# Kernel optimization log

Measured on AMD Instinct MI355X. Metric: run time of the kernel, lower is better.

## Reference

```python
import jax, jax.numpy as jnp
import numpy as np

N_NODES = 50000
N_EDGES = 300000
F_IN, HID, N_CLS = 256, 256, 128


def _glorot_linear(key, fan_in, fan_out):
    # torch.nn.Linear-style uniform init, kaiming bound 1/sqrt(fan_in)
    s = 1.0 / np.sqrt(fan_in)
    return jax.random.uniform(key, (fan_in, fan_out), jnp.float32, -s, s)


def setup_inputs() -> dict:
    key = jax.random.key(0)
    ks = jax.random.split(key, 8)
    x = jax.random.normal(ks[0], (N_NODES, F_IN), jnp.float32)
    edge_index = jax.random.randint(ks[1], (2, N_EDGES), 0, N_NODES, dtype=jnp.int32)
    return {
        "x": x,
        "edge_index": edge_index,
        "W1": _glorot_linear(ks[2], F_IN, HID), "b1": jnp.zeros((HID,), jnp.float32),
        "W2": _glorot_linear(ks[3], HID, HID),  "b2": jnp.zeros((HID,), jnp.float32),
        "W3": _glorot_linear(ks[4], HID, HID),  "b3": jnp.zeros((HID,), jnp.float32),
        "W4": _glorot_linear(ks[5], HID, N_CLS), "b4": jnp.zeros((N_CLS,), jnp.float32),
    }


def _gcn_conv(x, W, b, src, dst, norm, n):
    # x' = D^{-1/2} (A + I) D^{-1/2} X W + b   (PyG GCNConv default)
    h = x @ W                                  # [N, out]
    msg = h[src] * norm[:, None]               # gather + edge scaling  [E', out]
    return jax.ops.segment_sum(msg, dst, num_segments=n) + b


def reference(x, edge_index, W1, b1, W2, b2, W3, b3, W4, b4):
    n = x.shape[0]
    loops = jnp.arange(n, dtype=edge_index.dtype)
    src = jnp.concatenate([edge_index[0], loops])  # add self-loops
    dst = jnp.concatenate([edge_index[1], loops])
    # symmetric normalization: deg over target nodes (unit edge weights)
    deg = jax.ops.segment_sum(jnp.ones_like(dst, jnp.float32), dst, num_segments=n)
    dis = jnp.where(deg > 0, jax.lax.rsqrt(jnp.maximum(deg, 1.0)), 0.0)
    norm = dis[src] * dis[dst]                     # [E']

    h = jax.nn.relu(_gcn_conv(x, W1, b1, src, dst, norm, n))
    h = jax.nn.relu(_gcn_conv(h, W2, b2, src, dst, norm, n))
    h = jax.nn.relu(_gcn_conv(h, W3, b3, src, dst, norm, n))
    h = _gcn_conv(h, W4, b4, src, dst, norm, n)    # [N, C]

    # global_add_pool with batch == zeros -> single-graph sum pool
    pooled = jnp.sum(h, axis=0, keepdims=True)     # [1, C]
    return (pooled, jax.nn.log_softmax(pooled, axis=1))
```

## Files before the change

kernel.cpp:

```cpp
#include <hip/hip_runtime.h>


typedef __attribute__((ext_vector_type(8))) short short8;
typedef __attribute__((ext_vector_type(4))) float float4v;

__device__ __forceinline__ unsigned short f2b(float f) {
    unsigned int u = __builtin_bit_cast(unsigned int, f);
    u += 0x7fffu + ((u >> 16) & 1u);
    return (unsigned short)(u >> 16);
}
__device__ __forceinline__ float b2f(unsigned short b) {
    unsigned int u = ((unsigned int)b) << 16;
    return __builtin_bit_cast(float, u);
}


__global__ void zero_kernel(int* __restrict__ cnt, float* __restrict__ tsum,
                            float* __restrict__ acc, int N) {
    int i = blockIdx.x * 256 + threadIdx.x;
    if (i < N) { cnt[i] = 0; tsum[i] = 0.f; }
    if (i < 256) acc[i] = 0.f;
}

__global__ void count_kernel(const int* __restrict__ dst, int* __restrict__ cnt, int E) {
    int i = blockIdx.x * blockDim.x + threadIdx.x;
    if (i < E) atomicAdd(&cnt[dst[i]], 1);
}

__global__ void blocksum_kernel(const int* __restrict__ cnt, int* __restrict__ bsum, int N) {
    __shared__ int s[256];
    int t = threadIdx.x;
    int i = blockIdx.x * 256 + t;
    s[t] = (i < N) ? cnt[i] : 0;
    __syncthreads();
    for (int d = 128; d > 0; d >>= 1) {
        if (t < d) s[t] += s[t + d];
        __syncthreads();
    }
    if (t == 0) bsum[blockIdx.x] = s[0];
}

__global__ void bscan_kernel(int* __restrict__ bsum, int B) {
    __shared__ int s[256];
    int t = threadIdx.x;
    int v = (t < B) ? bsum[t] : 0;
    s[t] = v;
    __syncthreads();
    for (int d = 1; d < 256; d <<= 1) {
        int x = (t >= d) ? s[t - d] : 0;
        __syncthreads();
        s[t] += x;
        __syncthreads();
    }
    if (t < B) bsum[t] = s[t] - v;
}

__global__ void finalize_kernel(const int* __restrict__ cnt, const int* __restrict__ bsum,
                                int* __restrict__ offs, int* __restrict__ cursor,
                                float* __restrict__ dis, int N, int E) {
    __shared__ int s[256];
    int t = threadIdx.x;
    int i = blockIdx.x * 256 + t;
    int c = (i < N) ? cnt[i] : 0;
    s[t] = c;
    __syncthreads();
    for (int d = 1; d < 256; d <<= 1) {
        int x = (t >= d) ? s[t - d] : 0;
        __syncthreads();
        s[t] += x;
        __syncthreads();
    }
    if (i < N) {
        int ex = bsum[blockIdx.x] + s[t] - c;
        offs[i] = ex;
        cursor[i] = ex;
        dis[i] = rsqrtf((float)(c + 1));
    }
    if (blockIdx.x == 0 && t == 0) offs[N] = E;
}

__global__ void scatter_outsum_kernel(const int* __restrict__ src, const int* __restrict__ dst,
                                      const float* __restrict__ dis, int* __restrict__ cursor,
                                      int* __restrict__ csr_src, float* __restrict__ csr_nrm,
                                      float* __restrict__ tsum, int E) {
    int i = blockIdx.x * blockDim.x + threadIdx.x;
    if (i < E) {
        int s = src[i], d = dst[i];
        float dd = dis[d];
        int pos = atomicAdd(&cursor[d], 1);
        csr_src[pos] = s;
        csr_nrm[pos] = dis[s] * dd;
        atomicAdd(&tsum[s], dd);
    }
}


__global__ void convert_wt_kernel(const float* __restrict__ W1, const float* __restrict__ W2,
                                  const float* __restrict__ W3, unsigned short* __restrict__ Wt1,
                                  unsigned short* __restrict__ Wt2, unsigned short* __restrict__ Wt3) {
    const float* W = (blockIdx.y == 0) ? W1 : (blockIdx.y == 1) ? W2 : W3;
    unsigned short* Wt = (blockIdx.y == 0) ? Wt1 : (blockIdx.y == 1) ? Wt2 : Wt3;
    int n = blockIdx.x;
    int k = threadIdx.x;
    Wt[n * 256 + k] = f2b(W[k * 256 + n]);
}

template <int AFP32>
__global__ __launch_bounds__(512, 4) void gemm_bf16_kernel(
        const void* __restrict__ Ap, const unsigned short* __restrict__ Wt,
        unsigned short* __restrict__ C, int M) {
    __shared__ __align__(16) unsigned char smem[65536];
    unsigned short* As = (unsigned short*)smem;
    unsigned short* Bs = (unsigned short*)(smem + 128 * 72 * 2);
    const int tid = threadIdx.x;
    const int lane = tid & 63;
    const int wave = tid >> 6;
    const int l15 = lane & 15;
    const int quad = lane >> 4;
    const int wm = wave & 1;
    const int wn = wave >> 1;
    const int m0 = blockIdx.x * 128;

    float4v acc[4][4] = {};

    const int srow = tid >> 3;
    const int skof = (tid & 7) * 8;

    for (int kk = 0; kk < 256; kk += 64) {
#pragma unroll
        for (int p = 0; p < 2; p++) {
            int row = p * 64 + srow;
            int gm = m0 + row;
            if (AFP32) {
                const float* Af = (const float*)Ap;
                float4 lo = make_float4(0.f, 0.f, 0.f, 0.f);
                float4 hi = make_float4(0.f, 0.f, 0.f, 0.f);
                if (gm < M) {
                    lo = *(const float4*)&Af[(size_t)gm * 256 + kk + skof];
                    hi = *(const float4*)&Af[(size_t)gm * 256 + kk + skof + 4];
                }
                union { unsigned short u[8]; float4 v; } pk;
                pk.u[0] = f2b(lo.x); pk.u[1] = f2b(lo.y);
                pk.u[2] = f2b(lo.z); pk.u[3] = f2b(lo.w);
                pk.u[4] = f2b(hi.x); pk.u[5] = f2b(hi.y);
                pk.u[6] = f2b(hi.z); pk.u[7] = f2b(hi.w);
                *(float4*)&As[row * 72 + skof] = pk.v;
            } else {
                const unsigned short* Ab = (const unsigned short*)Ap;
                float4 av = make_float4(0.f, 0.f, 0.f, 0.f);
                if (gm < M) av = *(const float4*)&Ab[(size_t)gm * 256 + kk + skof];
                *(float4*)&As[row * 72 + skof] = av;
            }
        }
#pragma unroll
        for (int p = 0; p < 4; p++) {
            int row = p * 64 + srow;
            float4 bv = *(const float4*)&Wt[(size_t)row * 256 + kk + skof];
            *(float4*)&Bs[row * 72 + skof] = bv;
        }
        __syncthreads();
#pragma unroll
        for (int ks = 0; ks < 64; ks += 32) {
            short8 af[4], bf[4];
#pragma unroll
            for (int mi = 0; mi < 4; mi++)
                af[mi] = *(const short8*)&As[(wm * 64 + mi * 16 + l15) * 72 + ks + quad * 8];
#pragma unroll
            for (int nj = 0; nj < 4; nj++)
                bf[nj] = *(const short8*)&Bs[(wn * 64 + nj * 16 + l15) * 72 + ks + quad * 8];
#pragma unroll
            for (int mi = 0; mi < 4; mi++)
#pragma unroll
                for (int nj = 0; nj < 4; nj++)
                    acc[mi][nj] = __builtin_amdgcn_mfma_f32_16x16x32_bf16(
                        af[mi], bf[nj], acc[mi][nj], 0, 0, 0);
        }
        __syncthreads();
    }

    unsigned short* Cs = (unsigned short*)smem;
#pragma unroll
    for (int mi = 0; mi < 4; mi++)
#pragma unroll
        for (int r = 0; r < 4; r++) {
            int row = wm * 64 + mi * 16 + quad * 4 + r;
#pragma unroll
            for (int nj = 0; nj < 4; nj++)
                Cs[row * 256 + wn * 64 + nj * 16 + l15] = f2b(acc[mi][nj][r]);
        }
    __syncthreads();
#pragma unroll
    for (int i = 0; i < 8; i++) {
        int g = i * 512 + tid;
        int row = g >> 5;
        int c8 = (g & 31) * 8;
        if (m0 + row < M)
            *(float4*)&C[(size_t)(m0 + row) * 256 + c8] = *(const float4*)&Cs[row * 256 + c8];
    }
}

template <int RELU, int POOL>
__global__ __launch_bounds__(256) void agg_bf16_kernel(
        const unsigned short* __restrict__ T, const float* __restrict__ bias,
        const int* __restrict__ offs, const int* __restrict__ csr_src,
        const float* __restrict__ csr_nrm, const float* __restrict__ dis,
        unsigned short* __restrict__ out, int N,
        const float* __restrict__ tsum, float* __restrict__ partial) {
    int hw = threadIdx.x >> 5;
    int l = threadIdx.x & 31;
    int v = blockIdx.x * 8 + hw;
    int f8 = l * 8;
    float a[8] = {};
    float wv = 0.f;
    if (v < N) {
        int beg = offs[v], end = offs[v + 1];
        float dv = dis[v];
        float w = dv * dv;
        {
            short8 hs = *(const short8*)&T[(size_t)v * 256 + f8];
#pragma unroll
            for (int i = 0; i < 8; i++) a[i] = w * b2f((unsigned short)hs[i]);
        }
        int e = beg;
        for (; e + 4 <= end; e += 4) {
            int s0 = csr_src[e],     s1 = csr_src[e + 1];
            int s2 = csr_src[e + 2], s3 = csr_src[e + 3];
            float n0 = csr_nrm[e],     n1 = csr_nrm[e + 1];
            float n2 = csr_nrm[e + 2], n3 = csr_nrm[e + 3];
            short8 h0 = *(const short8*)&T[(size_t)s0 * 256 + f8];
            short8 h1 = *(const short8*)&T[(size_t)s1 * 256 + f8];
            short8 h2 = *(const short8*)&T[(size_t)s2 * 256 + f8];
            short8 h3 = *(const short8*)&T[(size_t)s3 * 256 + f8];
#pragma unroll
            for (int i = 0; i < 8; i++)
                a[i] += n0 * b2f((unsigned short)h0[i]) + n1 * b2f((unsigned short)h1[i])
                      + n2 * b2f((unsigned short)h2[i]) + n3 * b2f((unsigned short)h3[i]);
        }
        for (; e < end; e++) {
            int s = csr_src[e];
            float nm = csr_nrm[e];
            short8 h = *(const short8*)&T[(size_t)s * 256 + f8];
#pragma unroll
            for (int i = 0; i < 8; i++) a[i] += nm * b2f((unsigned short)h[i]);
        }
        float4 bv0 = *(const float4*)&bias[f8];
        float4 bv1 = *(const float4*)&bias[f8 + 4];
        a[0] += bv0.x; a[1] += bv0.y; a[2] += bv0.z; a[3] += bv0.w;
        a[4] += bv1.x; a[5] += bv1.y; a[6] += bv1.z; a[7] += bv1.w;
        if (RELU) {
#pragma unroll
            for (int i = 0; i < 8; i++) a[i] = fmaxf(a[i], 0.f);
        }
        uint4 o;
        o.x = (unsigned int)f2b(a[0]) | ((unsigned int)f2b(a[1]) << 16);
        o.y = (unsigned int)f2b(a[2]) | ((unsigned int)f2b(a[3]) << 16);
        o.z = (unsigned int)f2b(a[4]) | ((unsigned int)f2b(a[5]) << 16);
        o.w = (unsigned int)f2b(a[6]) | ((unsigned int)f2b(a[7]) << 16);
        *(uint4*)&out[(size_t)v * 256 + f8] = o;
        if (POOL) wv = dv * (dv + tsum[v]);
    }
    if (POOL) {
        __shared__ float red[2048];
#pragma unroll
        for (int i = 0; i < 8; i++) red[i * 256 + hw * 32 + l] = wv * a[i];
        __syncthreads();
        for (int s = 4; s > 0; s >>= 1) {
            if (hw < s) {
#pragma unroll
                for (int i = 0; i < 8; i++)
                    red[i * 256 + hw * 32 + l] += red[i * 256 + (hw + s) * 32 + l];
            }
            __syncthreads();
        }
        int f = threadIdx.x;
        partial[(size_t)blockIdx.x * 256 + f] = red[(f & 7) * 256 + (f >> 3)];
    }
}

__global__ void wpool_reduce(const float* __restrict__ partial, float* __restrict__ acc, int P) {
    int f = threadIdx.x;
    float a = 0.f;
    for (int p = blockIdx.x; p < P; p += gridDim.x)
        a += partial[(size_t)p * 256 + f];
    atomicAdd(&acc[f], a);
}

__global__ void final_kernel(const float* __restrict__ acc, const float* __restrict__ W4,
                             const float* __restrict__ b4, float* __restrict__ out, int N) {
    __shared__ float red[128];
    int c = threadIdx.x;
    float p = (float)N * b4[c];
    for (int k = 0; k < 256; k++) p += acc[k] * W4[k * 128 + c];
    out[c] = p;
    red[c] = p;
    __syncthreads();
    for (int s = 64; s > 0; s >>= 1) {
        if (c < s) red[c] = fmaxf(red[c], red[c + s]);
        __syncthreads();
    }
    float m = red[0];
    __syncthreads();
    red[c] = expf(p - m);
    __syncthreads();
    for (int s = 64; s > 0; s >>= 1) {
        if (c < s) red[c] += red[c + s];
        __syncthreads();
    }
    float lse = m + logf(red[0]);
    out[128 + c] = p - lse;
}

extern "C" void kernel_launch(void* const* d_in, const int* in_sizes, int n_in,
                              void* d_out, int out_size, void* d_ws, size_t ws_size,
                              hipStream_t stream) {
    const float* x  = (const float*)d_in[0];
    const int*   ei = (const int*)d_in[1];
    const float* W1 = (const float*)d_in[2];
    const float* b1 = (const float*)d_in[3];
    const float* W2 = (const float*)d_in[4];
    const float* b2 = (const float*)d_in[5];
    const float* W3 = (const float*)d_in[6];
    const float* b3 = (const float*)d_in[7];
    const float* W4 = (const float*)d_in[8];
    const float* b4 = (const float*)d_in[9];

    const int N = in_sizes[0] / 256;
    const int E = in_sizes[1] / 2;
    const int* src = ei;
    const int* dst = ei + E;

    char* p = (char*)d_ws;
    auto alloc = [&](size_t bytes) {
        char* r = p;
        p += (bytes + 255) & ~(size_t)255;
        return r;
    };
    int ab = (N + 7) / 8;

    int*            cnt     = (int*)alloc((size_t)N * 4);
    int*            offs    = (int*)alloc((size_t)(N + 1) * 4);
    int*            cursor  = (int*)alloc((size_t)N * 4);
    float*          dis     = (float*)alloc((size_t)N * 4);
    float*          tsum    = (float*)alloc((size_t)N * 4);
    int*            bsum    = (int*)alloc(1024 * 4);
    int*            csr_src = (int*)alloc((size_t)E * 4);
    float*          csr_nrm = (float*)alloc((size_t)E * 4);
    unsigned short* Wt1     = (unsigned short*)alloc(256 * 256 * 2);
    unsigned short* Wt2     = (unsigned short*)alloc(256 * 256 * 2);
    unsigned short* Wt3     = (unsigned short*)alloc(256 * 256 * 2);
    unsigned short* T       = (unsigned short*)alloc((size_t)N * 256 * 2);
    unsigned short* Abuf    = (unsigned short*)alloc((size_t)N * 256 * 2);
    float*          partial = (float*)alloc((size_t)ab * 256 * 4);
    float*          accbuf  = (float*)alloc(256 * 4);

    int eb = (E + 255) / 256;
    int nb = (N + 255) / 256;
    zero_kernel<<<nb, 256, 0, stream>>>(cnt, tsum, accbuf, N);
    count_kernel<<<eb, 256, 0, stream>>>(dst, cnt, E);
    blocksum_kernel<<<nb, 256, 0, stream>>>(cnt, bsum, N);
    bscan_kernel<<<1, 256, 0, stream>>>(bsum, nb);
    finalize_kernel<<<nb, 256, 0, stream>>>(cnt, bsum, offs, cursor, dis, N, E);
    scatter_outsum_kernel<<<eb, 256, 0, stream>>>(src, dst, dis, cursor, csr_src,
                                                  csr_nrm, tsum, E);

    convert_wt_kernel<<<dim3(256, 3), 256, 0, stream>>>(W1, W2, W3, Wt1, Wt2, Wt3);

    int ggrid = (N + 127) / 128;
    gemm_bf16_kernel<1><<<ggrid, 512, 0, stream>>>(x, Wt1, T, N);
    agg_bf16_kernel<1, 0><<<ab, 256, 0, stream>>>(T, b1, offs, csr_src, csr_nrm, dis,
                                                  Abuf, N, nullptr, nullptr);
    gemm_bf16_kernel<0><<<ggrid, 512, 0, stream>>>(Abuf, Wt2, T, N);
    agg_bf16_kernel<1, 0><<<ab, 256, 0, stream>>>(T, b2, offs, csr_src, csr_nrm, dis,
                                                  Abuf, N, nullptr, nullptr);
    gemm_bf16_kernel<0><<<ggrid, 512, 0, stream>>>(Abuf, Wt3, T, N);
    agg_bf16_kernel<1, 1><<<ab, 256, 0, stream>>>(T, b3, offs, csr_src, csr_nrm, dis,
                                                  Abuf, N, tsum, partial);

    wpool_reduce<<<64, 256, 0, stream>>>(partial, accbuf, ab);
    final_kernel<<<1, 128, 0, stream>>>(accbuf, W4, b4, (float*)d_out, N);
}
```

Measured before the change: 351.2 us.

## Split GEMM over N into 128x128 tiles with 256-thread blocks and direct stores

The GEMM now tiles the output as 128x128 per block, adding a second grid dimension over output columns and using 256 threads (4 waves) instead of 512. This shrinks shared memory from 64KB to about 36KB to allow more resident blocks. The LDS-staged coalesced epilogue is dropped in favour of direct scalar bf16 stores from the accumulators. The cost is that the A tile is loaded twice (once per column block), and the output writes are narrower and less coalesced.

New measurement: 358.6 us. 2.1% more time.

```diff
diff --git a/kernel.cpp b/kernel.cpp
--- a/kernel.cpp
+++ b/kernel.cpp
@@ -106,12 +106,11 @@
 }
 
 template <int AFP32>
-__global__ __launch_bounds__(512, 4) void gemm_bf16_kernel(
+__global__ __launch_bounds__(256, 3) void gemm_bf16_kernel(
         const void* __restrict__ Ap, const unsigned short* __restrict__ Wt,
         unsigned short* __restrict__ C, int M) {
-    __shared__ __align__(16) unsigned char smem[65536];
-    unsigned short* As = (unsigned short*)smem;
-    unsigned short* Bs = (unsigned short*)(smem + 128 * 72 * 2);
+    __shared__ unsigned short As[128 * 72];
+    __shared__ unsigned short Bs[128 * 72];
     const int tid = threadIdx.x;
     const int lane = tid & 63;
     const int wave = tid >> 6;
@@ -120,6 +119,7 @@
     const int wm = wave & 1;
     const int wn = wave >> 1;
     const int m0 = blockIdx.x * 128;
+    const int n0 = blockIdx.y * 128;
 
     float4v acc[4][4] = {};
 
@@ -128,8 +128,8 @@
 
     for (int kk = 0; kk < 256; kk += 64) {
 #pragma unroll
-        for (int p = 0; p < 2; p++) {
-            int row = p * 64 + srow;
+        for (int p = 0; p < 4; p++) {
+            int row = p * 32 + srow;
             int gm = m0 + row;
             if (AFP32) {
                 const float* Af = (const float*)Ap;
@@ -151,11 +151,7 @@
                 if (gm < M) av = *(const float4*)&Ab[(size_t)gm * 256 + kk + skof];
                 *(float4*)&As[row * 72 + skof] = av;
             }
-        }
-#pragma unroll
-        for (int p = 0; p < 4; p++) {
-            int row = p * 64 + srow;
-            float4 bv = *(const float4*)&Wt[(size_t)row * 256 + kk + skof];
+            float4 bv = *(const float4*)&Wt[(size_t)(n0 + row) * 256 + kk + skof];
             *(float4*)&Bs[row * 72 + skof] = bv;
         }
         __syncthreads();
@@ -178,24 +174,19 @@
         __syncthreads();
     }
 
-    unsigned short* Cs = (unsigned short*)smem;
-#pragma unroll
-    for (int mi = 0; mi < 4; mi++)
+#pragma unroll
+    for (int mi = 0; mi < 4; mi++) {
 #pragma unroll
         for (int r = 0; r < 4; r++) {
-            int row = wm * 64 + mi * 16 + quad * 4 + r;
-#pragma unroll
-            for (int nj = 0; nj < 4; nj++)
-                Cs[row * 256 + wn * 64 + nj * 16 + l15] = f2b(acc[mi][nj][r]);
-        }
-    __syncthreads();
-#pragma unroll
-    for (int i = 0; i < 8; i++) {
-        int g = i * 512 + tid;
-        int row = g >> 5;
-        int c8 = (g & 31) * 8;
-        if (m0 + row < M)
-            *(float4*)&C[(size_t)(m0 + row) * 256 + c8] = *(const float4*)&Cs[row * 256 + c8];
+            int row = m0 + wm * 64 + mi * 16 + quad * 4 + r;
+            if (row < M) {
+#pragma unroll
+                for (int nj = 0; nj < 4; nj++) {
+                    int col = n0 + wn * 64 + nj * 16 + l15;
+                    C[(size_t)row * 256 + col] = f2b(acc[mi][nj][r]);
+                }
+            }
+        }
     }
 }
 
@@ -365,14 +356,14 @@
 
     convert_wt_kernel<<<dim3(256, 3), 256, 0, stream>>>(W1, W2, W3, Wt1, Wt2, Wt3);
 
-    int ggrid = (N + 127) / 128;
-    gemm_bf16_kernel<1><<<ggrid, 512, 0, stream>>>(x, Wt1, T, N);
+    dim3 ggrid((N + 127) / 128, 2);
+    gemm_bf16_kernel<1><<<ggrid, 256, 0, stream>>>(x, Wt1, T, N);
     agg_bf16_kernel<1, 0><<<ab, 256, 0, stream>>>(T, b1, offs, csr_src, csr_nrm, dis,
                                                   Abuf, N, nullptr, nullptr);
-    gemm_bf16_kernel<0><<<ggrid, 512, 0, stream>>>(Abuf, Wt2, T, N);
+    gemm_bf16_kernel<0><<<ggrid, 256, 0, stream>>>(Abuf, Wt2, T, N);
     agg_bf16_kernel<1, 0><<<ab, 256, 0, stream>>>(T, b2, offs, csr_src, csr_nrm, dis,
                                                   Abuf, N, nullptr, nullptr);
-    gemm_bf16_kernel<0><<<ggrid, 512, 0, stream>>>(Abuf, Wt3, T, N);
+    gemm_bf16_kernel<0><<<ggrid, 256, 0, stream>>>(Abuf, Wt3, T, N);
     agg_bf16_kernel<1, 1><<<ab, 256, 0, stream>>>(T, b3, offs, csr_src, csr_nrm, dis,
                                                   Abuf, N, tsum, partial);
 
```
